# Optimization experiments

Measured on AMD Instinct MI355X. Metric: run time of the kernel, lower is better.

## Reference

```python
import jax, jax.numpy as jnp
import numpy as np

B, T, D = 4, 50, 512
SRC, SENTS, WORDS = 400, 16, 40
NEG = jnp.float32(-1e30)  # stands in for -inf mask fill (numerically identical post-softmax)


def _seq_mask(lengths, max_len):
    # [n, max_len] bool, True where position < length
    return jnp.arange(max_len)[None, :] < lengths[:, None]


def _mlp_score(q, h, Wq, bq, Uc, v):
    # Bahdanau additive score: v^T tanh(W q + U h)
    # q: [b,t,d], h: [b,s,d] -> [b,t,s]
    wq = q @ Wq + bq                       # [b,t,d]
    uh = h @ Uc                            # [b,s,d]
    wquh = jnp.tanh(wq[:, :, None, :] + uh[:, None, :, :])  # [b,t,s,d]
    return jnp.einsum('btsd,d->bts', wquh, v)


def setup_inputs() -> dict:
    key = jax.random.key(0)
    ks = jax.random.split(key, 20)
    s = np.float32(1.0 / np.sqrt(D))
    def p(k, shape):
        return jax.random.normal(k, shape, jnp.float32) * s
    return {
        'source': jax.random.normal(ks[0], (B, T, D), jnp.float32),
        'src_bank': jax.random.normal(ks[1], (SRC, B, D), jnp.float32),
        'src_lengths': jax.random.randint(ks[2], (B,), 1, SRC + 1),
        'qa_sent_bank': jax.random.normal(ks[3], (SENTS, B, D), jnp.float32),
        'qa_sent_lengths': jax.random.randint(ks[4], (B,), 1, SENTS + 1),
        'qa_word_bank': jax.random.normal(ks[5], (WORDS, B, SENTS, D), jnp.float32),
        'qa_word_lengths': jax.random.randint(ks[6], (B, SENTS), 1, WORDS + 1),
        'Wq_word': p(ks[7], (D, D)), 'bq_word': jnp.zeros((D,), jnp.float32),
        'Uc_word': p(ks[8], (D, D)), 'v_word': p(ks[9], (D,)),
        'Wq_sent': p(ks[10], (D, D)), 'bq_sent': jnp.zeros((D,), jnp.float32),
        'Uc_sent': p(ks[11], (D, D)), 'v_sent': p(ks[12], (D,)),
        'Wq_pass': p(ks[13], (D, D)), 'bq_pass': jnp.zeros((D,), jnp.float32),
        'Uc_pass': p(ks[14], (D, D)), 'v_pass': p(ks[15], (D,)),
    }


def _forward(source, src_bank, qa_sent_bank, qa_word_bank,
             Wq_word, bq_word, Uc_word, v_word,
             Wq_sent, bq_sent, Uc_sent, v_sent,
             Wq_pass, bq_pass, Uc_pass, v_pass,
             src_lengths, qa_word_lengths):
    b = source.shape[0]
    # [words,b,sents,d] -> [b,sents,words,d] -> [b, sents*words, d]
    qa_word = jnp.transpose(qa_word_bank, (1, 2, 0, 3)).reshape(b, SENTS * WORDS, D)
    src = jnp.transpose(src_bank, (1, 0, 2))       # [b,src,d]
    sent = jnp.transpose(qa_sent_bank, (1, 0, 2))  # [b,sents,d]

    qa_word_align = _mlp_score(source, qa_word, Wq_word, bq_word, Uc_word, v_word)  # [b,t,sents*words]
    src_align = _mlp_score(source, src, Wq_pass, bq_pass, Uc_pass, v_pass)          # [b,t,src]
    qa_sent_align = _mlp_score(source, sent, Wq_sent, bq_sent, Uc_sent, v_sent)     # [b,t,sents]

    # hierarchical combination: word score scaled by its sentence score
    qa_hier = (qa_word_align.reshape(b, T, SENTS, WORDS)
               * qa_sent_align[..., None]).reshape(b, T, SENTS * WORDS)

    align = jnp.concatenate([src_align, qa_hier], axis=-1)  # [b,t,src+sents*words]

    qa_mask = _seq_mask(qa_word_lengths.reshape(-1), WORDS).reshape(b, SENTS * WORDS)[:, None, :]
    src_mask = _seq_mask(src_lengths, SRC)[:, None, :]
    mask = jnp.concatenate([src_mask, qa_mask], axis=-1)

    align = jnp.where(mask, align, NEG)
    align_vectors = jax.nn.softmax(align, axis=-1)  # joint length-masked softmax

    memory = jnp.concatenate([src, qa_word], axis=1)          # [b, src+sents*words, d]
    c = jnp.einsum('bts,bsd->btd', align_vectors, memory)     # weighted context sum
    return c


def reference(source, src_bank, src_lengths, qa_sent_bank, qa_sent_lengths,
              qa_word_bank, qa_word_lengths,
              Wq_word, bq_word, Uc_word, v_word,
              Wq_sent, bq_sent, Uc_sent, v_sent,
              Wq_pass, bq_pass, Uc_pass, v_pass):
    # qa_sent_lengths is accepted but unused, matching the original forward()
    return _forward(source, src_bank, qa_sent_bank, qa_word_bank,
                    Wq_word, bq_word, Uc_word, v_word,
                    Wq_sent, bq_sent, Uc_sent, v_sent,
                    Wq_pass, bq_pass, Uc_pass, v_pass,
                    src_lengths, qa_word_lengths)
```

## Files before the change

kernel.cpp:

```cpp
#include <hip/hip_runtime.h>
#include <hip/hip_bf16.h>


#define B_    4
#define T_    50
#define D_    512
#define SRC_  400
#define SENTS_ 16
#define WORDS_ 40
#define NW_   640
#define NMEM_ 1040
#define NK_   1056
#define NJOB_ 1056

#define C2L2E 2.8853900817779268f

typedef unsigned short ushort_t;
using s8v = __attribute__((ext_vector_type(8))) short;
using f4v = __attribute__((ext_vector_type(4))) float;

#define OFF_WQ_WORD 0
#define OFF_WQ_SENT 102400
#define OFF_WQ_PASS 204800
#define OFF_UH_SRC  307200
#define OFF_UH_WORD 1126400
#define OFF_UH_SENT 2437120
#define OFF_SC_SRC  2469888
#define OFF_SC_WORD 2549888
#define OFF_SC_SENT 2677888
#define P_BYTE_OFF  10724352ull
#define MT_BYTE_OFF 11265024ull
#define WT_BYTE_OFF 15590400ull

__device__ __forceinline__ ushort_t f2b(float f) {
    __hip_bfloat16 h = __float2bfloat16(f);
    return *(ushort_t*)&h;
}

__global__ __launch_bounds__(256) void k0f_transpose(
    const float* __restrict__ w0, const float* __restrict__ w1,
    const float* __restrict__ w2, const float* __restrict__ w3,
    const float* __restrict__ w4, const float* __restrict__ w5,
    const float* __restrict__ src_bank, const float* __restrict__ qa_word_bank,
    ushort_t* __restrict__ wt, ushort_t* __restrict__ mt)
{
    __shared__ float tile[32][33];
    int bid = blockIdx.x;
    int tx = threadIdx.x & 31, ty = threadIdx.x >> 5;
    if (bid < 1536) {
        int z = bid >> 8, r = bid & 255;
        int n0 = (r & 15) * 32, k0 = (r >> 4) * 32;
        const float* W;
        switch (z) {
            case 0: W = w0; break; case 1: W = w1; break; case 2: W = w2; break;
            case 3: W = w3; break; case 4: W = w4; break; default: W = w5; break;
        }
        ushort_t* Wt = wt + z * (D_ * D_);
#pragma unroll
        for (int a = 0; a < 4; ++a)
            tile[ty + a * 8][tx] = W[(k0 + ty + a * 8) * D_ + n0 + tx];
        __syncthreads();
#pragma unroll
        for (int a = 0; a < 4; ++a)
            Wt[(n0 + ty + a * 8) * D_ + k0 + tx] = f2b(tile[tx][ty + a * 8]);
    } else {
        int tb = bid - 1536;
        int b = tb / 528, r = tb - b * 528;
        int s0 = (r % 33) * 32, d0 = (r / 33) * 32;
#pragma unroll
        for (int a = 0; a < 4; ++a) {
            int s = s0 + ty + a * 8;
            float val = 0.f;
            if (s < SRC_) {
                val = src_bank[(s * B_ + b) * D_ + d0 + tx];
            } else if (s < NMEM_) {
                int j = s - SRC_; int se = j / WORDS_; int wd = j - se * WORDS_;
                val = qa_word_bank[((wd * B_ + b) * SENTS_ + se) * D_ + d0 + tx];
            }
            tile[ty + a * 8][tx] = val;
        }
        __syncthreads();
        ushort_t* base = mt + (size_t)b * D_ * NK_;
#pragma unroll
        for (int a = 0; a < 4; ++a) {
            int d = d0 + ty + a * 8;
            base[(size_t)d * NK_ + s0 + tx] = f2b(tile[tx][ty + a * 8]);
        }
    }
}

__global__ __launch_bounds__(256) void k1_gemm(
    const float* __restrict__ source, const float* __restrict__ src_bank,
    const float* __restrict__ qa_sent_bank, const float* __restrict__ qa_word_bank,
    const ushort_t* __restrict__ wt,
    const float* __restrict__ bq_word, const float* __restrict__ bq_sent,
    const float* __restrict__ bq_pass,
    float* __restrict__ wsf)
{
    __shared__ short At[64 * 32];
    __shared__ short Bt[64 * 32];
    int bid = blockIdx.x;
    int z, rem;
    if (bid < 96)       { z = bid >> 5; rem = bid & 31; }
    else if (bid < 416) { z = 3; rem = bid - 96; }
    else if (bid < 616) { z = 4; rem = bid - 416; }
    else                { z = 5; rem = bid - 616; }
    int by = rem >> 3, bx = rem & 7;
    int M, atype; const float* bias; float* C;
    switch (z) {
        case 0: M = 200;  atype = 0; bias = bq_word; C = wsf + OFF_WQ_WORD; break;
        case 1: M = 200;  atype = 0; bias = bq_sent; C = wsf + OFF_WQ_SENT; break;
        case 2: M = 200;  atype = 0; bias = bq_pass; C = wsf + OFF_WQ_PASS; break;
        case 3: M = 2560; atype = 1; bias = nullptr; C = wsf + OFF_UH_WORD; break;
        case 4: M = 1600; atype = 2; bias = nullptr; C = wsf + OFF_UH_SRC;  break;
        default: M = 64;  atype = 3; bias = nullptr; C = wsf + OFF_UH_SENT; break;
    }
    int m0 = by * 64, n0 = bx * 64;
    const ushort_t* W = wt + z * (D_ * D_);

    int tid = threadIdx.x;
    int lane = tid & 63, wv = tid >> 6;
    int quad = lane >> 4, l16 = lane & 15;
    int sm = tid >> 2, koff = (tid & 3) * 8;

    const float* arow = nullptr;
    {
        int r = m0 + sm;
        if (r < M) {
            if (atype == 0) arow = source + r * D_;
            else if (atype == 1) { int b = r / NW_; int j = r - b * NW_;
                                   int se = j / WORDS_; int wd = j - se * WORDS_;
                                   arow = qa_word_bank + ((wd * B_ + b) * SENTS_ + se) * D_; }
            else if (atype == 2) { int b = r / SRC_; int j = r - b * SRC_;
                                   arow = src_bank + (j * B_ + b) * D_; }
            else                 { int b = r >> 4; int s2 = r & 15;
                                   arow = qa_sent_bank + (s2 * B_ + b) * D_; }
        }
    }
    const ushort_t* wrow = W + (n0 + sm) * D_;

    auto loadA = [&](float* r, int kk) {
        if (arow) {
            float4 f0 = *(const float4*)(arow + kk * 32 + koff);
            float4 f1 = *(const float4*)(arow + kk * 32 + koff + 4);
            r[0]=f0.x; r[1]=f0.y; r[2]=f0.z; r[3]=f0.w;
            r[4]=f1.x; r[5]=f1.y; r[6]=f1.z; r[7]=f1.w;
        } else {
#pragma unroll
            for (int i = 0; i < 8; ++i) r[i] = 0.f;
        }
    };

    f4v acc[4] = { {0.f,0.f,0.f,0.f}, {0.f,0.f,0.f,0.f},
                   {0.f,0.f,0.f,0.f}, {0.f,0.f,0.f,0.f} };

    float a0[8], a1[8];
    int4 w0v, w1v;
    loadA(a0, 0); w0v = *(const int4*)(wrow + 0 * 32 + koff);
    loadA(a1, 1); w1v = *(const int4*)(wrow + 1 * 32 + koff);

    for (int kk = 0; kk < 16; ++kk) {
        union { ushort_t u[8]; int4 v; } pk;
#pragma unroll
        for (int i = 0; i < 8; ++i) pk.u[i] = f2b(a0[i]);
        *(int4*)(At + sm * 32 + koff) = pk.v;
        *(int4*)(Bt + sm * 32 + koff) = w0v;
        __syncthreads();
#pragma unroll
        for (int i = 0; i < 8; ++i) a0[i] = a1[i];
        w0v = w1v;
        if (kk < 14) {
            loadA(a1, kk + 2);
            w1v = *(const int4*)(wrow + (kk + 2) * 32 + koff);
        }
        s8v af = *(const s8v*)(At + (wv * 16 + l16) * 32 + quad * 8);
#pragma unroll
        for (int ng = 0; ng < 4; ++ng) {
            s8v bf = *(const s8v*)(Bt + (ng * 16 + l16) * 32 + quad * 8);
            acc[ng] = __builtin_amdgcn_mfma_f32_16x16x32_bf16(af, bf, acc[ng], 0, 0, 0);
        }
        __syncthreads();
    }
#pragma unroll
    for (int ng = 0; ng < 4; ++ng) {
        int col = n0 + ng * 16 + l16;
        float bb = bias ? bias[col] : 0.f;
#pragma unroll
        for (int rr = 0; rr < 4; ++rr) {
            int row = m0 + wv * 16 + quad * 4 + rr;
            if (row < M) C[row * D_ + col] = (acc[ng][rr] + bb) * C2L2E;
        }
    }
}

__global__ __launch_bounds__(256) void k2_scores(
    const float* __restrict__ v_word, const float* __restrict__ v_sent,
    const float* __restrict__ v_pass,
    const int* __restrict__ src_lengths, const int* __restrict__ qa_word_lengths,
    float* __restrict__ wsf)
{
    int lane = threadIdx.x & 63;
    int job2 = blockIdx.x * 4 + (threadIdx.x >> 6);
    int job = job2 >> 1, th = job2 & 1;
    int b = job / NJOB_, slot = job - b * NJOB_;
    const float* uh; const float* v; const float* wq; float* out; int ostride;
    if (slot < SRC_) {
        if (slot >= src_lengths[b]) return;
        uh = wsf + OFF_UH_SRC + (b * SRC_ + slot) * D_;
        v = v_pass; wq = wsf + OFF_WQ_PASS + b * T_ * D_;
        out = wsf + OFF_SC_SRC + b * T_ * SRC_ + slot; ostride = SRC_;
    } else if (slot < NMEM_) {
        int j = slot - SRC_;
        int se = j / WORDS_; int wd = j - se * WORDS_;
        if (wd >= qa_word_lengths[b * SENTS_ + se]) return;
        uh = wsf + OFF_UH_WORD + (b * NW_ + j) * D_;
        v = v_word; wq = wsf + OFF_WQ_WORD + b * T_ * D_;
        out = wsf + OFF_SC_WORD + b * T_ * NW_ + j; ostride = NW_;
    } else {
        int s2 = slot - NMEM_;
        uh = wsf + OFF_UH_SENT + (b * SENTS_ + s2) * D_;
        v = v_sent; wq = wsf + OFF_WQ_SENT + b * T_ * D_;
        out = wsf + OFF_SC_SENT + b * T_ * SENTS_ + s2; ostride = SENTS_;
    }
    int d0 = lane * 8;
    float4 u0 = *(const float4*)(uh + d0);
    float4 u1 = *(const float4*)(uh + d0 + 4);
    float uhr[8] = {u0.x, u0.y, u0.z, u0.w, u1.x, u1.y, u1.z, u1.w};
    float4 v0 = *(const float4*)(v + d0);
    float4 v1 = *(const float4*)(v + d0 + 4);
    float vr[8] = {v0.x, v0.y, v0.z, v0.w, v1.x, v1.y, v1.z, v1.w};

    float vs = ((vr[0] + vr[1]) + (vr[2] + vr[3])) + ((vr[4] + vr[5]) + (vr[6] + vr[7]));
#pragma unroll
    for (int off = 32; off > 0; off >>= 1) vs += __shfl_xor(vs, off, 64);

    const float* wqh = wq + th * 25 * D_;
#pragma unroll 1
    for (int g = 0; g < 5; ++g) {
        float a5[5];
#pragma unroll
        for (int u5 = 0; u5 < 5; ++u5) {
            const float* wr = wqh + (g * 5 + u5) * D_ + d0;
            float4 w0 = *(const float4*)(wr);
            float4 w1 = *(const float4*)(wr + 4);
            float wrr[8] = {w0.x, w0.y, w0.z, w0.w, w1.x, w1.y, w1.z, w1.w};
            float a = 0.f;
#pragma unroll
            for (int j = 0; j < 8; ++j) {
                float e = __builtin_amdgcn_exp2f(wrr[j] + uhr[j]);
                float r = __builtin_amdgcn_rcpf(e + 1.f);
                a = fmaf(vr[j], r, a);
            }
            a5[u5] = a;
        }
#pragma unroll
        for (int off = 32; off > 0; off >>= 1) {
#pragma unroll
            for (int u5 = 0; u5 < 5; ++u5) a5[u5] += __shfl_xor(a5[u5], off, 64);
        }
        if (lane == 0) {
#pragma unroll
            for (int u5 = 0; u5 < 5; ++u5)
                out[(th * 25 + g * 5 + u5) * ostride] = fmaf(-2.f, a5[u5], vs);
        }
    }
}

__global__ __launch_bounds__(256) void k3a_softmax(
    const int* __restrict__ src_lengths, const int* __restrict__ qa_word_lengths,
    const float* __restrict__ wsf, ushort_t* __restrict__ P)
{
    __shared__ float p[NMEM_];
    __shared__ float red[4];
    int tid = threadIdx.x, lane = tid & 63, wv = tid >> 6;
    int bt = blockIdx.x, b = bt / T_, t = bt - b * T_;
    const float* sc_src  = wsf + OFF_SC_SRC  + bt * SRC_;
    const float* sc_word = wsf + OFF_SC_WORD + bt * NW_;
    const float* sc_sent = wsf + OFF_SC_SENT + bt * SENTS_;
    int slen = src_lengths[b];
    float mx = -3.0e38f;
    for (int j = tid; j < NMEM_; j += 256) {
        float val;
        if (j < SRC_) {
            val = (j < slen) ? sc_src[j] : -1e30f;
        } else {
            int jj = j - SRC_; int se = jj / WORDS_; int wd = jj - se * WORDS_;
            float raw = sc_word[jj] * sc_sent[se];
            val = (wd < qa_word_lengths[b * SENTS_ + se]) ? raw : -1e30f;
        }
        p[j] = val;
        mx = fmaxf(mx, val);
    }
#pragma unroll
    for (int off = 32; off > 0; off >>= 1) mx = fmaxf(mx, __shfl_xor(mx, off, 64));
    if (lane == 0) red[wv] = mx;
    __syncthreads();
    mx = fmaxf(fmaxf(red[0], red[1]), fmaxf(red[2], red[3]));
    __syncthreads();
    float lsum = 0.f;
    for (int j = tid; j < NMEM_; j += 256) {
        float e = __expf(p[j] - mx);
        p[j] = e; lsum += e;
    }
#pragma unroll
    for (int off = 32; off > 0; off >>= 1) lsum += __shfl_xor(lsum, off, 64);
    if (lane == 0) red[wv] = lsum;
    __syncthreads();
    float inv = 1.f / (red[0] + red[1] + red[2] + red[3]);
    ushort_t* prow = P + (size_t)(b * 64 + t) * NK_;
    for (int j = tid; j < NK_; j += 256)
        prow[j] = (j < NMEM_) ? f2b(p[j] * inv) : (ushort_t)0;
}

__global__ __launch_bounds__(256) void k3c_gemm(
    const ushort_t* __restrict__ P, const ushort_t* __restrict__ Mt,
    float* __restrict__ out)
{
    __shared__ short At[64 * 32];
    __shared__ short Bt[32 * 32];
    int b = blockIdx.y;
    int n0 = blockIdx.x * 32;
    int tid = threadIdx.x;
    int lane = tid & 63, wv = tid >> 6;
    int quad = lane >> 4, l16 = lane & 15;
    int smA = tid >> 2, koffA = (tid & 3) * 8;
    int smB = tid >> 3, koffB = (tid & 7) * 4;

    const ushort_t* arow = P + (size_t)(b * 64 + smA) * NK_ + koffA;
    const ushort_t* brow = Mt + ((size_t)(b * D_ + n0 + smB)) * NK_ + koffB;

    f4v acc[2] = { {0.f,0.f,0.f,0.f}, {0.f,0.f,0.f,0.f} };

    int4 a0 = *(const int4*)(arow);
    int2 b0 = *(const int2*)(brow);
    int4 a1 = *(const int4*)(arow + 32);
    int2 b1 = *(const int2*)(brow + 32);
    int4 a2 = *(const int4*)(arow + 64);
    int2 b2 = *(const int2*)(brow + 64);

    for (int kk = 0; kk < 33; ++kk) {
        *(int4*)(At + smA * 32 + koffA) = a0;
        *(int2*)(Bt + smB * 32 + koffB) = b0;
        __syncthreads();
        a0 = a1; a1 = a2; b0 = b1; b1 = b2;
        if (kk < 30) {
            a2 = *(const int4*)(arow + (kk + 3) * 32);
            b2 = *(const int2*)(brow + (kk + 3) * 32);
        }
        s8v af = *(const s8v*)(At + (wv * 16 + l16) * 32 + quad * 8);
#pragma unroll
        for (int ng = 0; ng < 2; ++ng) {
            s8v bf = *(const s8v*)(Bt + (ng * 16 + l16) * 32 + quad * 8);
            acc[ng] = __builtin_amdgcn_mfma_f32_16x16x32_bf16(af, bf, acc[ng], 0, 0, 0);
        }
        __syncthreads();
    }
#pragma unroll
    for (int ng = 0; ng < 2; ++ng) {
        int col = n0 + ng * 16 + l16;
#pragma unroll
        for (int rr = 0; rr < 4; ++rr) {
            int row = wv * 16 + quad * 4 + rr;
            if (row < T_) out[(size_t)(b * T_ + row) * D_ + col] = acc[ng][rr];
        }
    }
}

extern "C" void kernel_launch(void* const* d_in, const int* in_sizes, int n_in,
                              void* d_out, int out_size, void* d_ws, size_t ws_size,
                              hipStream_t stream)
{
    (void)in_sizes; (void)n_in; (void)out_size; (void)ws_size;
    const float* source          = (const float*)d_in[0];
    const float* src_bank        = (const float*)d_in[1];
    const int*   src_lengths     = (const int*)d_in[2];
    const float* qa_sent_bank    = (const float*)d_in[3];
    const float* qa_word_bank    = (const float*)d_in[5];
    const int*   qa_word_lengths = (const int*)d_in[6];
    const float* Wq_word = (const float*)d_in[7];
    const float* bq_word = (const float*)d_in[8];
    const float* Uc_word = (const float*)d_in[9];
    const float* v_word  = (const float*)d_in[10];
    const float* Wq_sent = (const float*)d_in[11];
    const float* bq_sent = (const float*)d_in[12];
    const float* Uc_sent = (const float*)d_in[13];
    const float* v_sent  = (const float*)d_in[14];
    const float* Wq_pass = (const float*)d_in[15];
    const float* bq_pass = (const float*)d_in[16];
    const float* Uc_pass = (const float*)d_in[17];
    const float* v_pass  = (const float*)d_in[18];

    float* wsf = (float*)d_ws;
    ushort_t* Pb  = (ushort_t*)((char*)d_ws + P_BYTE_OFF);
    ushort_t* mt  = (ushort_t*)((char*)d_ws + MT_BYTE_OFF);
    ushort_t* wt  = (ushort_t*)((char*)d_ws + WT_BYTE_OFF);
    float* out = (float*)d_out;

    k0f_transpose<<<dim3(3648), dim3(256), 0, stream>>>(
        Wq_word, Wq_sent, Wq_pass, Uc_word, Uc_pass, Uc_sent,
        src_bank, qa_word_bank, wt, mt);
    k1_gemm<<<dim3(624), dim3(256), 0, stream>>>(
        source, src_bank, qa_sent_bank, qa_word_bank, wt,
        bq_word, bq_sent, bq_pass, wsf);
    k2_scores<<<dim3(NJOB_ * 2), dim3(256), 0, stream>>>(
        v_word, v_sent, v_pass, src_lengths, qa_word_lengths, wsf);
    k3a_softmax<<<dim3(200), dim3(256), 0, stream>>>(src_lengths, qa_word_lengths, wsf, Pb);
    k3c_gemm<<<dim3(16, 4), dim3(256), 0, stream>>>(Pb, mt, out);
}
```

Before: 154.7 us.

## Fuse additive-attention scoring with masked softmax into one per-query kernel

Merges the score kernel and the softmax kernel into one kernel with one 512-thread block per (batch, query) row. The Wq vectors and v are held in registers, and each block computes scores for all memory slots straight into shared memory. This removes the global round trip of the score arrays and one launch. The trade-off is that parallelism changes from 2112 blocks parallel over memory slots to 200 blocks parallel over queries. Each uh row is now re-read by 50 blocks instead of once per half-T, which relies on L2 reuse.

```diff
diff --git a/kernel.cpp b/kernel.cpp
--- a/kernel.cpp
+++ b/kernel.cpp
@@ -11,7 +11,6 @@
 #define NW_   640
 #define NMEM_ 1040
 #define NK_   1056
-#define NJOB_ 1056
 
 #define C2L2E 2.8853900817779268f
 
@@ -25,9 +24,6 @@
 #define OFF_UH_SRC  307200
 #define OFF_UH_WORD 1126400
 #define OFF_UH_SENT 2437120
-#define OFF_SC_SRC  2469888
-#define OFF_SC_WORD 2549888
-#define OFF_SC_SENT 2677888
 #define P_BYTE_OFF  10724352ull
 #define MT_BYTE_OFF 11265024ull
 #define WT_BYTE_OFF 15590400ull
@@ -193,112 +189,138 @@
     }
 }
 
-__global__ __launch_bounds__(256) void k2_scores(
+__global__ __launch_bounds__(512) void k2s_scores_softmax(
     const float* __restrict__ v_word, const float* __restrict__ v_sent,
     const float* __restrict__ v_pass,
-    const int* __restrict__ src_lengths, const int* __restrict__ qa_word_lengths,
-    float* __restrict__ wsf)
-{
-    int lane = threadIdx.x & 63;
-    int job2 = blockIdx.x * 4 + (threadIdx.x >> 6);
-    int job = job2 >> 1, th = job2 & 1;
-    int b = job / NJOB_, slot = job - b * NJOB_;
-    const float* uh; const float* v; const float* wq; float* out; int ostride;
-    if (slot < SRC_) {
-        if (slot >= src_lengths[b]) return;
-        uh = wsf + OFF_UH_SRC + (b * SRC_ + slot) * D_;
-        v = v_pass; wq = wsf + OFF_WQ_PASS + b * T_ * D_;
-        out = wsf + OFF_SC_SRC + b * T_ * SRC_ + slot; ostride = SRC_;
-    } else if (slot < NMEM_) {
-        int j = slot - SRC_;
-        int se = j / WORDS_; int wd = j - se * WORDS_;
-        if (wd >= qa_word_lengths[b * SENTS_ + se]) return;
-        uh = wsf + OFF_UH_WORD + (b * NW_ + j) * D_;
-        v = v_word; wq = wsf + OFF_WQ_WORD + b * T_ * D_;
-        out = wsf + OFF_SC_WORD + b * T_ * NW_ + j; ostride = NW_;
-    } else {
-        int s2 = slot - NMEM_;
-        uh = wsf + OFF_UH_SENT + (b * SENTS_ + s2) * D_;
-        v = v_sent; wq = wsf + OFF_WQ_SENT + b * T_ * D_;
-        out = wsf + OFF_SC_SENT + b * T_ * SENTS_ + s2; ostride = SENTS_;
-    }
-    int d0 = lane * 8;
-    float4 u0 = *(const float4*)(uh + d0);
-    float4 u1 = *(const float4*)(uh + d0 + 4);
-    float uhr[8] = {u0.x, u0.y, u0.z, u0.w, u1.x, u1.y, u1.z, u1.w};
-    float4 v0 = *(const float4*)(v + d0);
-    float4 v1 = *(const float4*)(v + d0 + 4);
-    float vr[8] = {v0.x, v0.y, v0.z, v0.w, v1.x, v1.y, v1.z, v1.w};
-
-    float vs = ((vr[0] + vr[1]) + (vr[2] + vr[3])) + ((vr[4] + vr[5]) + (vr[6] + vr[7]));
-#pragma unroll
-    for (int off = 32; off > 0; off >>= 1) vs += __shfl_xor(vs, off, 64);
-
-    const float* wqh = wq + th * 25 * D_;
-#pragma unroll 1
-    for (int g = 0; g < 5; ++g) {
-        float a5[5];
-#pragma unroll
-        for (int u5 = 0; u5 < 5; ++u5) {
-            const float* wr = wqh + (g * 5 + u5) * D_ + d0;
-            float4 w0 = *(const float4*)(wr);
-            float4 w1 = *(const float4*)(wr + 4);
-            float wrr[8] = {w0.x, w0.y, w0.z, w0.w, w1.x, w1.y, w1.z, w1.w};
-            float a = 0.f;
-#pragma unroll
-            for (int j = 0; j < 8; ++j) {
-                float e = __builtin_amdgcn_exp2f(wrr[j] + uhr[j]);
-                float r = __builtin_amdgcn_rcpf(e + 1.f);
-                a = fmaf(vr[j], r, a);
-            }
-            a5[u5] = a;
-        }
-#pragma unroll
-        for (int off = 32; off > 0; off >>= 1) {
-#pragma unroll
-            for (int u5 = 0; u5 < 5; ++u5) a5[u5] += __shfl_xor(a5[u5], off, 64);
-        }
-        if (lane == 0) {
-#pragma unroll
-            for (int u5 = 0; u5 < 5; ++u5)
-                out[(th * 25 + g * 5 + u5) * ostride] = fmaf(-2.f, a5[u5], vs);
-        }
-    }
-}
-
-__global__ __launch_bounds__(256) void k3a_softmax(
     const int* __restrict__ src_lengths, const int* __restrict__ qa_word_lengths,
     const float* __restrict__ wsf, ushort_t* __restrict__ P)
 {
     __shared__ float p[NMEM_];
-    __shared__ float red[4];
+    __shared__ float sentL[SENTS_];
+    __shared__ float red[8];
+    __shared__ int lensL[SENTS_];
     int tid = threadIdx.x, lane = tid & 63, wv = tid >> 6;
     int bt = blockIdx.x, b = bt / T_, t = bt - b * T_;
-    const float* sc_src  = wsf + OFF_SC_SRC  + bt * SRC_;
-    const float* sc_word = wsf + OFF_SC_WORD + bt * NW_;
-    const float* sc_sent = wsf + OFF_SC_SENT + bt * SENTS_;
     int slen = src_lengths[b];
+    int d0 = lane * 8;
+
+    for (int j = tid; j < NMEM_; j += 512) p[j] = -1e30f;
+    if (tid < SENTS_) lensL[tid] = qa_word_lengths[b * SENTS_ + tid];
+
+    float wqp[8], wqw[8], wqs[8], vp[8], vw[8], vs8[8];
+    {
+        const float* qp = wsf + OFF_WQ_PASS + (size_t)bt * D_ + d0;
+        const float* qw = wsf + OFF_WQ_WORD + (size_t)bt * D_ + d0;
+        const float* qs = wsf + OFF_WQ_SENT + (size_t)bt * D_ + d0;
+        float4 f;
+        f = *(const float4*)(qp);     wqp[0]=f.x; wqp[1]=f.y; wqp[2]=f.z; wqp[3]=f.w;
+        f = *(const float4*)(qp + 4); wqp[4]=f.x; wqp[5]=f.y; wqp[6]=f.z; wqp[7]=f.w;
+        f = *(const float4*)(qw);     wqw[0]=f.x; wqw[1]=f.y; wqw[2]=f.z; wqw[3]=f.w;
+        f = *(const float4*)(qw + 4); wqw[4]=f.x; wqw[5]=f.y; wqw[6]=f.z; wqw[7]=f.w;
+        f = *(const float4*)(qs);     wqs[0]=f.x; wqs[1]=f.y; wqs[2]=f.z; wqs[3]=f.w;
+        f = *(const float4*)(qs + 4); wqs[4]=f.x; wqs[5]=f.y; wqs[6]=f.z; wqs[7]=f.w;
+        f = *(const float4*)(v_pass + d0);     vp[0]=f.x; vp[1]=f.y; vp[2]=f.z; vp[3]=f.w;
+        f = *(const float4*)(v_pass + d0 + 4); vp[4]=f.x; vp[5]=f.y; vp[6]=f.z; vp[7]=f.w;
+        f = *(const float4*)(v_word + d0);     vw[0]=f.x; vw[1]=f.y; vw[2]=f.z; vw[3]=f.w;
+        f = *(const float4*)(v_word + d0 + 4); vw[4]=f.x; vw[5]=f.y; vw[6]=f.z; vw[7]=f.w;
+        f = *(const float4*)(v_sent + d0);     vs8[0]=f.x; vs8[1]=f.y; vs8[2]=f.z; vs8[3]=f.w;
+        f = *(const float4*)(v_sent + d0 + 4); vs8[4]=f.x; vs8[5]=f.y; vs8[6]=f.z; vs8[7]=f.w;
+    }
+    float Vp = ((vp[0]+vp[1])+(vp[2]+vp[3])) + ((vp[4]+vp[5])+(vp[6]+vp[7]));
+    float Vw = ((vw[0]+vw[1])+(vw[2]+vw[3])) + ((vw[4]+vw[5])+(vw[6]+vw[7]));
+    float Vs = ((vs8[0]+vs8[1])+(vs8[2]+vs8[3])) + ((vs8[4]+vs8[5])+(vs8[6]+vs8[7]));
+#pragma unroll
+    for (int off = 32; off > 0; off >>= 1) {
+        Vp += __shfl_xor(Vp, off, 64);
+        Vw += __shfl_xor(Vw, off, 64);
+        Vs += __shfl_xor(Vs, off, 64);
+    }
+
+    auto part8 = [&](const float* uh, const float* wq8, const float* v8) -> float {
+        float4 u0 = *(const float4*)(uh);
+        float4 u1 = *(const float4*)(uh + 4);
+        float ur[8] = {u0.x, u0.y, u0.z, u0.w, u1.x, u1.y, u1.z, u1.w};
+        float a = 0.f;
+#pragma unroll
+        for (int j = 0; j < 8; ++j) {
+            float e = __builtin_amdgcn_exp2f(wq8[j] + ur[j]);
+            float r = __builtin_amdgcn_rcpf(e + 1.f);
+            a = fmaf(v8[j], r, a);
+        }
+        return a;
+    };
+
+    {
+        int s0 = wv * 2;
+        const float* uh = wsf + OFF_UH_SENT + (size_t)(b * SENTS_ + s0) * D_ + d0;
+        float a0 = part8(uh, wqs, vs8);
+        float a1 = part8(uh + D_, wqs, vs8);
+#pragma unroll
+        for (int off = 32; off > 0; off >>= 1) {
+            a0 += __shfl_xor(a0, off, 64);
+            a1 += __shfl_xor(a1, off, 64);
+        }
+        if (lane == 0) {
+            sentL[s0]     = fmaf(-2.f, a0, Vs);
+            sentL[s0 + 1] = fmaf(-2.f, a1, Vs);
+        }
+    }
+    __syncthreads();
+
+    for (int c = wv; c < 208; c += 8) {
+        int j0 = c * 5;
+        float a[5];
+        if (j0 < SRC_) {
+            if (j0 >= slen) continue;
+            const float* uh = wsf + OFF_UH_SRC + (size_t)(b * SRC_ + j0) * D_ + d0;
+#pragma unroll
+            for (int u = 0; u < 5; ++u) a[u] = part8(uh + u * D_, wqp, vp);
+#pragma unroll
+            for (int off = 32; off > 0; off >>= 1) {
+#pragma unroll
+                for (int u = 0; u < 5; ++u) a[u] += __shfl_xor(a[u], off, 64);
+            }
+            if (lane == 0) {
+#pragma unroll
+                for (int u = 0; u < 5; ++u)
+                    if (j0 + u < slen) p[j0 + u] = fmaf(-2.f, a[u], Vp);
+            }
+        } else {
+            int jw = j0 - SRC_;
+            int se = jw / WORDS_;
+            int wd0 = jw - se * WORDS_;
+            int lim = lensL[se];
+            if (wd0 >= lim) continue;
+            const float* uh = wsf + OFF_UH_WORD + (size_t)(b * NW_ + jw) * D_ + d0;
+            float sse = sentL[se];
+#pragma unroll
+            for (int u = 0; u < 5; ++u) a[u] = part8(uh + u * D_, wqw, vw);
+#pragma unroll
+            for (int off = 32; off > 0; off >>= 1) {
+#pragma unroll
+                for (int u = 0; u < 5; ++u) a[u] += __shfl_xor(a[u], off, 64);
+            }
+            if (lane == 0) {
+#pragma unroll
+                for (int u = 0; u < 5; ++u)
+                    if (wd0 + u < lim)
+                        p[SRC_ + jw + u] = fmaf(-2.f, a[u], Vw) * sse;
+            }
+        }
+    }
+    __syncthreads();
+
     float mx = -3.0e38f;
-    for (int j = tid; j < NMEM_; j += 256) {
-        float val;
-        if (j < SRC_) {
-            val = (j < slen) ? sc_src[j] : -1e30f;
-        } else {
-            int jj = j - SRC_; int se = jj / WORDS_; int wd = jj - se * WORDS_;
-            float raw = sc_word[jj] * sc_sent[se];
-            val = (wd < qa_word_lengths[b * SENTS_ + se]) ? raw : -1e30f;
-        }
-        p[j] = val;
-        mx = fmaxf(mx, val);
-    }
+    for (int j = tid; j < NMEM_; j += 512) mx = fmaxf(mx, p[j]);
 #pragma unroll
     for (int off = 32; off > 0; off >>= 1) mx = fmaxf(mx, __shfl_xor(mx, off, 64));
     if (lane == 0) red[wv] = mx;
     __syncthreads();
-    mx = fmaxf(fmaxf(red[0], red[1]), fmaxf(red[2], red[3]));
+    mx = fmaxf(fmaxf(fmaxf(red[0], red[1]), fmaxf(red[2], red[3])),
+               fmaxf(fmaxf(red[4], red[5]), fmaxf(red[6], red[7])));
     __syncthreads();
     float lsum = 0.f;
-    for (int j = tid; j < NMEM_; j += 256) {
+    for (int j = tid; j < NMEM_; j += 512) {
         float e = __expf(p[j] - mx);
         p[j] = e; lsum += e;
     }
@@ -306,9 +328,10 @@
     for (int off = 32; off > 0; off >>= 1) lsum += __shfl_xor(lsum, off, 64);
     if (lane == 0) red[wv] = lsum;
     __syncthreads();
-    float inv = 1.f / (red[0] + red[1] + red[2] + red[3]);
+    float inv = 1.f / (((red[0] + red[1]) + (red[2] + red[3])) +
+                       ((red[4] + red[5]) + (red[6] + red[7])));
     ushort_t* prow = P + (size_t)(b * 64 + t) * NK_;
-    for (int j = tid; j < NK_; j += 256)
+    for (int j = tid; j < NK_; j += 512)
         prow[j] = (j < NMEM_) ? f2b(p[j] * inv) : (ushort_t)0;
 }
 
@@ -402,8 +425,7 @@
     k1_gemm<<<dim3(624), dim3(256), 0, stream>>>(
         source, src_bank, qa_sent_bank, qa_word_bank, wt,
         bq_word, bq_sent, bq_pass, wsf);
-    k2_scores<<<dim3(NJOB_ * 2), dim3(256), 0, stream>>>(
-        v_word, v_sent, v_pass, src_lengths, qa_word_lengths, wsf);
-    k3a_softmax<<<dim3(200), dim3(256), 0, stream>>>(src_lengths, qa_word_lengths, wsf, Pb);
+    k2s_scores_softmax<<<dim3(200), dim3(512), 0, stream>>>(
+        v_word, v_sent, v_pass, src_lengths, qa_word_lengths, wsf, Pb);
     k3c_gemm<<<dim3(16, 4), dim3(256), 0, stream>>>(Pb, mt, out);
 }
```

New measurement: 164.4 us. +6.2%, slower.

## Batch four memory slots per wave in scores; split-K final GEMM across waves

Applied to the files above, without the earlier changes.

The score kernel now has each wave handle four consecutive memory slots, so every Wq row loaded from global memory is reused across four uh vectors. The grid shrinks to a quarter of its former size. The final P·M GEMM splits the K dimension across the four waves. Each wave stages its own tiles without block barriers and computes all 64 rows, then partial results are reduced through shared memory. This adds register pressure and a shared-memory reduction in exchange for fewer loads and syncs.

```diff
diff --git a/kernel.cpp b/kernel.cpp
--- a/kernel.cpp
+++ b/kernel.cpp
@@ -11,7 +11,6 @@
 #define NW_   640
 #define NMEM_ 1040
 #define NK_   1056
-#define NJOB_ 1056
 
 #define C2L2E 2.8853900817779268f
 
@@ -200,32 +199,45 @@
     float* __restrict__ wsf)
 {
     int lane = threadIdx.x & 63;
-    int job2 = blockIdx.x * 4 + (threadIdx.x >> 6);
-    int job = job2 >> 1, th = job2 & 1;
-    int b = job / NJOB_, slot = job - b * NJOB_;
-    const float* uh; const float* v; const float* wq; float* out; int ostride;
-    if (slot < SRC_) {
-        if (slot >= src_lengths[b]) return;
-        uh = wsf + OFF_UH_SRC + (b * SRC_ + slot) * D_;
+    int jid = blockIdx.x * 4 + (threadIdx.x >> 6);
+    int b = jid / 528, r = jid - b * 528;
+    int th = r & 1, grp = r >> 1;
+    const float* uhb; const float* v; const float* wq; float* outb; int ostride;
+    int nact;
+    if (grp < 100) {
+        int slot0 = grp * 4;
+        int slen = src_lengths[b];
+        if (slot0 >= slen) return;
+        nact = min(4, slen - slot0);
+        uhb = wsf + OFF_UH_SRC + (size_t)(b * SRC_ + slot0) * D_;
         v = v_pass; wq = wsf + OFF_WQ_PASS + b * T_ * D_;
-        out = wsf + OFF_SC_SRC + b * T_ * SRC_ + slot; ostride = SRC_;
-    } else if (slot < NMEM_) {
-        int j = slot - SRC_;
-        int se = j / WORDS_; int wd = j - se * WORDS_;
-        if (wd >= qa_word_lengths[b * SENTS_ + se]) return;
-        uh = wsf + OFF_UH_WORD + (b * NW_ + j) * D_;
+        outb = wsf + OFF_SC_SRC + b * T_ * SRC_ + slot0; ostride = SRC_;
+    } else if (grp < 260) {
+        int g = grp - 100; int se = g / 10; int wd0 = (g - se * 10) * 4;
+        int lim = qa_word_lengths[b * SENTS_ + se];
+        if (wd0 >= lim) return;
+        nact = min(4, lim - wd0);
+        int jw = se * WORDS_ + wd0;
+        uhb = wsf + OFF_UH_WORD + (size_t)(b * NW_ + jw) * D_;
         v = v_word; wq = wsf + OFF_WQ_WORD + b * T_ * D_;
-        out = wsf + OFF_SC_WORD + b * T_ * NW_ + j; ostride = NW_;
+        outb = wsf + OFF_SC_WORD + b * T_ * NW_ + jw; ostride = NW_;
     } else {
-        int s2 = slot - NMEM_;
-        uh = wsf + OFF_UH_SENT + (b * SENTS_ + s2) * D_;
+        int s0 = (grp - 260) * 4;
+        nact = 4;
+        uhb = wsf + OFF_UH_SENT + (size_t)(b * SENTS_ + s0) * D_;
         v = v_sent; wq = wsf + OFF_WQ_SENT + b * T_ * D_;
-        out = wsf + OFF_SC_SENT + b * T_ * SENTS_ + s2; ostride = SENTS_;
+        outb = wsf + OFF_SC_SENT + b * T_ * SENTS_ + s0; ostride = SENTS_;
     }
     int d0 = lane * 8;
-    float4 u0 = *(const float4*)(uh + d0);
-    float4 u1 = *(const float4*)(uh + d0 + 4);
-    float uhr[8] = {u0.x, u0.y, u0.z, u0.w, u1.x, u1.y, u1.z, u1.w};
+
+    float uhr[4][8];
+#pragma unroll
+    for (int u = 0; u < 4; ++u) {
+        float4 f0 = *(const float4*)(uhb + u * D_ + d0);
+        float4 f1 = *(const float4*)(uhb + u * D_ + d0 + 4);
+        uhr[u][0]=f0.x; uhr[u][1]=f0.y; uhr[u][2]=f0.z; uhr[u][3]=f0.w;
+        uhr[u][4]=f1.x; uhr[u][5]=f1.y; uhr[u][6]=f1.z; uhr[u][7]=f1.w;
+    }
     float4 v0 = *(const float4*)(v + d0);
     float4 v1 = *(const float4*)(v + d0 + 4);
     float vr[8] = {v0.x, v0.y, v0.z, v0.w, v1.x, v1.y, v1.z, v1.w};
@@ -234,34 +246,44 @@
 #pragma unroll
     for (int off = 32; off > 0; off >>= 1) vs += __shfl_xor(vs, off, 64);
 
-    const float* wqh = wq + th * 25 * D_;
+    const float* wqh = wq + th * 25 * D_ + d0;
 #pragma unroll 1
     for (int g = 0; g < 5; ++g) {
-        float a5[5];
-#pragma unroll
-        for (int u5 = 0; u5 < 5; ++u5) {
-            const float* wr = wqh + (g * 5 + u5) * D_ + d0;
+        float a[4][5];
+#pragma unroll
+        for (int t5 = 0; t5 < 5; ++t5) {
+            const float* wr = wqh + (g * 5 + t5) * D_;
             float4 w0 = *(const float4*)(wr);
             float4 w1 = *(const float4*)(wr + 4);
             float wrr[8] = {w0.x, w0.y, w0.z, w0.w, w1.x, w1.y, w1.z, w1.w};
-            float a = 0.f;
-#pragma unroll
-            for (int j = 0; j < 8; ++j) {
-                float e = __builtin_amdgcn_exp2f(wrr[j] + uhr[j]);
-                float r = __builtin_amdgcn_rcpf(e + 1.f);
-                a = fmaf(vr[j], r, a);
+#pragma unroll
+            for (int u = 0; u < 4; ++u) {
+                float acc = 0.f;
+#pragma unroll
+                for (int j = 0; j < 8; ++j) {
+                    float e = __builtin_amdgcn_exp2f(wrr[j] + uhr[u][j]);
+                    float rc = __builtin_amdgcn_rcpf(e + 1.f);
+                    acc = fmaf(vr[j], rc, acc);
+                }
+                a[u][t5] = acc;
             }
-            a5[u5] = a;
         }
 #pragma unroll
         for (int off = 32; off > 0; off >>= 1) {
 #pragma unroll
-            for (int u5 = 0; u5 < 5; ++u5) a5[u5] += __shfl_xor(a5[u5], off, 64);
+            for (int u = 0; u < 4; ++u)
+#pragma unroll
+                for (int t5 = 0; t5 < 5; ++t5)
+                    a[u][t5] += __shfl_xor(a[u][t5], off, 64);
         }
         if (lane == 0) {
 #pragma unroll
-            for (int u5 = 0; u5 < 5; ++u5)
-                out[(th * 25 + g * 5 + u5) * ostride] = fmaf(-2.f, a5[u5], vs);
+            for (int t5 = 0; t5 < 5; ++t5) {
+                int trow = (th * 25 + g * 5 + t5) * ostride;
+#pragma unroll
+                for (int u = 0; u < 4; ++u)
+                    if (u < nact) outb[trow + u] = fmaf(-2.f, a[u][t5], vs);
+            }
         }
     }
 }
@@ -316,53 +338,80 @@
     const ushort_t* __restrict__ P, const ushort_t* __restrict__ Mt,
     float* __restrict__ out)
 {
-    __shared__ short At[64 * 32];
-    __shared__ short Bt[32 * 32];
+    __shared__ short AtW[4][64 * 32];
+    __shared__ short BtW[4][32 * 32];
+    __shared__ float Cred[4][64 * 32];
     int b = blockIdx.y;
     int n0 = blockIdx.x * 32;
     int tid = threadIdx.x;
-    int lane = tid & 63, wv = tid >> 6;
+    int lane = tid & 63, w = tid >> 6;
     int quad = lane >> 4, l16 = lane & 15;
-    int smA = tid >> 2, koffA = (tid & 3) * 8;
-    int smB = tid >> 3, koffB = (tid & 7) * 4;
-
-    const ushort_t* arow = P + (size_t)(b * 64 + smA) * NK_ + koffA;
-    const ushort_t* brow = Mt + ((size_t)(b * D_ + n0 + smB)) * NK_ + koffB;
-
-    f4v acc[2] = { {0.f,0.f,0.f,0.f}, {0.f,0.f,0.f,0.f} };
-
-    int4 a0 = *(const int4*)(arow);
-    int2 b0 = *(const int2*)(brow);
-    int4 a1 = *(const int4*)(arow + 32);
-    int2 b1 = *(const int2*)(brow + 32);
-    int4 a2 = *(const int4*)(arow + 64);
-    int2 b2 = *(const int2*)(brow + 64);
-
-    for (int kk = 0; kk < 33; ++kk) {
-        *(int4*)(At + smA * 32 + koffA) = a0;
-        *(int2*)(Bt + smB * 32 + koffB) = b0;
-        __syncthreads();
-        a0 = a1; a1 = a2; b0 = b1; b1 = b2;
-        if (kk < 30) {
-            a2 = *(const int4*)(arow + (kk + 3) * 32);
-            b2 = *(const int2*)(brow + (kk + 3) * 32);
-        }
-        s8v af = *(const s8v*)(At + (wv * 16 + l16) * 32 + quad * 8);
-#pragma unroll
-        for (int ng = 0; ng < 2; ++ng) {
-            s8v bf = *(const s8v*)(Bt + (ng * 16 + l16) * 32 + quad * 8);
-            acc[ng] = __builtin_amdgcn_mfma_f32_16x16x32_bf16(af, bf, acc[ng], 0, 0, 0);
-        }
-        __syncthreads();
-    }
-#pragma unroll
-    for (int ng = 0; ng < 2; ++ng) {
-        int col = n0 + ng * 16 + l16;
-#pragma unroll
-        for (int rr = 0; rr < 4; ++rr) {
-            int row = wv * 16 + quad * 4 + rr;
-            if (row < T_) out[(size_t)(b * T_ + row) * D_ + col] = acc[ng][rr];
-        }
+
+    int ks = (w == 0) ? 0 : 9 + (w - 1) * 8;
+    int ke = ks + ((w == 0) ? 9 : 8);
+
+    const ushort_t* arow = P + (size_t)(b * 64 + lane) * NK_;
+    const ushort_t* brow = Mt + (size_t)(b * D_ + n0 + (lane >> 1)) * NK_ + (lane & 1) * 16;
+    short* At = AtW[w];
+    short* Bt = BtW[w];
+    short* atd = At + lane * 32;
+    short* btd = Bt + (lane >> 1) * 32 + (lane & 1) * 16;
+
+    f4v acc[4][2];
+#pragma unroll
+    for (int mi = 0; mi < 4; ++mi)
+#pragma unroll
+        for (int ng = 0; ng < 2; ++ng) acc[mi][ng] = f4v{0.f, 0.f, 0.f, 0.f};
+
+    int4 pa0 = *(const int4*)(arow + ks * 32);
+    int4 pa1 = *(const int4*)(arow + ks * 32 + 8);
+    int4 pa2 = *(const int4*)(arow + ks * 32 + 16);
+    int4 pa3 = *(const int4*)(arow + ks * 32 + 24);
+    int4 pb0 = *(const int4*)(brow + ks * 32);
+    int4 pb1 = *(const int4*)(brow + ks * 32 + 8);
+
+    for (int kk = ks; kk < ke; ++kk) {
+        *(int4*)(atd)      = pa0;
+        *(int4*)(atd + 8)  = pa1;
+        *(int4*)(atd + 16) = pa2;
+        *(int4*)(atd + 24) = pa3;
+        *(int4*)(btd)      = pb0;
+        *(int4*)(btd + 8)  = pb1;
+        if (kk + 1 < ke) {
+            pa0 = *(const int4*)(arow + (kk + 1) * 32);
+            pa1 = *(const int4*)(arow + (kk + 1) * 32 + 8);
+            pa2 = *(const int4*)(arow + (kk + 1) * 32 + 16);
+            pa3 = *(const int4*)(arow + (kk + 1) * 32 + 24);
+            pb0 = *(const int4*)(brow + (kk + 1) * 32);
+            pb1 = *(const int4*)(brow + (kk + 1) * 32 + 8);
+        }
+#pragma unroll
+        for (int mi = 0; mi < 4; ++mi) {
+            s8v af = *(const s8v*)(At + (mi * 16 + l16) * 32 + quad * 8);
+#pragma unroll
+            for (int ng = 0; ng < 2; ++ng) {
+                s8v bf = *(const s8v*)(Bt + (ng * 16 + l16) * 32 + quad * 8);
+                acc[mi][ng] = __builtin_amdgcn_mfma_f32_16x16x32_bf16(af, bf, acc[mi][ng], 0, 0, 0);
+            }
+        }
+    }
+
+#pragma unroll
+    for (int mi = 0; mi < 4; ++mi)
+#pragma unroll
+        for (int ng = 0; ng < 2; ++ng)
+#pragma unroll
+            for (int rr = 0; rr < 4; ++rr)
+                Cred[w][(mi * 16 + quad * 4 + rr) * 32 + ng * 16 + l16] = acc[mi][ng][rr];
+    __syncthreads();
+
+    int i0 = tid * 8;
+#pragma unroll
+    for (int e = 0; e < 8; ++e) {
+        int idx = i0 + e;
+        int row = idx >> 5, col = idx & 31;
+        float s = ((Cred[0][idx] + Cred[1][idx]) + (Cred[2][idx] + Cred[3][idx]));
+        if (row < T_) out[(size_t)(b * T_ + row) * D_ + n0 + col] = s;
     }
 }
 
@@ -402,7 +451,7 @@
     k1_gemm<<<dim3(624), dim3(256), 0, stream>>>(
         source, src_bank, qa_sent_bank, qa_word_bank, wt,
         bq_word, bq_sent, bq_pass, wsf);
-    k2_scores<<<dim3(NJOB_ * 2), dim3(256), 0, stream>>>(
+    k2_scores<<<dim3(528), dim3(256), 0, stream>>>(
         v_word, v_sent, v_pass, src_lengths, qa_word_lengths, wsf);
     k3a_softmax<<<dim3(200), dim3(256), 0, stream>>>(src_lengths, qa_word_lengths, wsf, Pb);
     k3c_gemm<<<dim3(16, 4), dim3(256), 0, stream>>>(Pb, mt, out);
```

Measured after the change: 167.7 us. 1.08x slower.

## Stage shared query rows in LDS and process four memory slots per block

Applied to the files above, without the earlier changes.

Regroups the additive-score kernel so each block handles four consecutive memory slots for the same batch and query half. The 25 query rows are copied once into shared memory and reused by the four waves, instead of each wave streaming them from global memory. This cuts redundant L2/global traffic on the wq rows. In exchange, each block uses about 50KB of LDS, which reduces occupancy, and adds a block barrier.

```diff
diff --git a/kernel.cpp b/kernel.cpp
--- a/kernel.cpp
+++ b/kernel.cpp
@@ -11,7 +11,6 @@
 #define NW_   640
 #define NMEM_ 1040
 #define NK_   1056
-#define NJOB_ 1056
 
 #define C2L2E 2.8853900817779268f
 
@@ -199,30 +198,52 @@
     const int* __restrict__ src_lengths, const int* __restrict__ qa_word_lengths,
     float* __restrict__ wsf)
 {
-    int lane = threadIdx.x & 63;
-    int job2 = blockIdx.x * 4 + (threadIdx.x >> 6);
-    int job = job2 >> 1, th = job2 & 1;
-    int b = job / NJOB_, slot = job - b * NJOB_;
-    const float* uh; const float* v; const float* wq; float* out; int ostride;
-    if (slot < SRC_) {
-        if (slot >= src_lengths[b]) return;
-        uh = wsf + OFF_UH_SRC + (b * SRC_ + slot) * D_;
-        v = v_pass; wq = wsf + OFF_WQ_PASS + b * T_ * D_;
-        out = wsf + OFF_SC_SRC + b * T_ * SRC_ + slot; ostride = SRC_;
-    } else if (slot < NMEM_) {
-        int j = slot - SRC_;
-        int se = j / WORDS_; int wd = j - se * WORDS_;
-        if (wd >= qa_word_lengths[b * SENTS_ + se]) return;
-        uh = wsf + OFF_UH_WORD + (b * NW_ + j) * D_;
-        v = v_word; wq = wsf + OFF_WQ_WORD + b * T_ * D_;
-        out = wsf + OFF_SC_WORD + b * T_ * NW_ + j; ostride = NW_;
+    __shared__ float wqL[25 * D_];
+    int tid = threadIdx.x, lane = tid & 63, wv = tid >> 6;
+    int bid = blockIdx.x;
+    int b = bid / 528, r = bid - b * 528;
+    int th = r & 1, grp = r >> 1;
+
+    const float* uhb; const float* v; const float* wqb; float* outb; int ostride;
+    int nact;
+    if (grp < 100) {
+        int slot0 = grp * 4;
+        int slen = src_lengths[b];
+        if (slot0 >= slen) return;
+        nact = min(4, slen - slot0);
+        uhb = wsf + OFF_UH_SRC + (size_t)(b * SRC_ + slot0) * D_;
+        v = v_pass; wqb = wsf + OFF_WQ_PASS + b * T_ * D_;
+        outb = wsf + OFF_SC_SRC + b * T_ * SRC_ + slot0; ostride = SRC_;
+    } else if (grp < 260) {
+        int g = grp - 100; int se = g / 10; int wd0 = (g - se * 10) * 4;
+        int lim = qa_word_lengths[b * SENTS_ + se];
+        if (wd0 >= lim) return;
+        nact = min(4, lim - wd0);
+        int jw = se * WORDS_ + wd0;
+        uhb = wsf + OFF_UH_WORD + (size_t)(b * NW_ + jw) * D_;
+        v = v_word; wqb = wsf + OFF_WQ_WORD + b * T_ * D_;
+        outb = wsf + OFF_SC_WORD + b * T_ * NW_ + jw; ostride = NW_;
     } else {
-        int s2 = slot - NMEM_;
-        uh = wsf + OFF_UH_SENT + (b * SENTS_ + s2) * D_;
-        v = v_sent; wq = wsf + OFF_WQ_SENT + b * T_ * D_;
-        out = wsf + OFF_SC_SENT + b * T_ * SENTS_ + s2; ostride = SENTS_;
-    }
+        int s0 = (grp - 260) * 4;
+        nact = 4;
+        uhb = wsf + OFF_UH_SENT + (size_t)(b * SENTS_ + s0) * D_;
+        v = v_sent; wqb = wsf + OFF_WQ_SENT + b * T_ * D_;
+        outb = wsf + OFF_SC_SENT + b * T_ * SENTS_ + s0; ostride = SENTS_;
+    }
+
+    {
+        const float4* src4 = (const float4*)(wqb + th * 25 * D_);
+        float4* dst4 = (float4*)wqL;
+#pragma unroll
+        for (int i = 0; i < 12; ++i) dst4[tid + i * 256] = src4[tid + i * 256];
+        if (tid < 128) dst4[tid + 3072] = src4[tid + 3072];
+    }
+    __syncthreads();
+
+    int u = wv;
+    if (u >= nact) return;
     int d0 = lane * 8;
+    const float* uh = uhb + u * D_;
     float4 u0 = *(const float4*)(uh + d0);
     float4 u1 = *(const float4*)(uh + d0 + 4);
     float uhr[8] = {u0.x, u0.y, u0.z, u0.w, u1.x, u1.y, u1.z, u1.w};
@@ -234,13 +255,14 @@
 #pragma unroll
     for (int off = 32; off > 0; off >>= 1) vs += __shfl_xor(vs, off, 64);
 
-    const float* wqh = wq + th * 25 * D_;
+    float* outw = outb + u;
+    const float* wl = wqL + d0;
 #pragma unroll 1
     for (int g = 0; g < 5; ++g) {
         float a5[5];
 #pragma unroll
         for (int u5 = 0; u5 < 5; ++u5) {
-            const float* wr = wqh + (g * 5 + u5) * D_ + d0;
+            const float* wr = wl + (g * 5 + u5) * D_;
             float4 w0 = *(const float4*)(wr);
             float4 w1 = *(const float4*)(wr + 4);
             float wrr[8] = {w0.x, w0.y, w0.z, w0.w, w1.x, w1.y, w1.z, w1.w};
@@ -248,8 +270,8 @@
 #pragma unroll
             for (int j = 0; j < 8; ++j) {
                 float e = __builtin_amdgcn_exp2f(wrr[j] + uhr[j]);
-                float r = __builtin_amdgcn_rcpf(e + 1.f);
-                a = fmaf(vr[j], r, a);
+                float rc = __builtin_amdgcn_rcpf(e + 1.f);
+                a = fmaf(vr[j], rc, a);
             }
             a5[u5] = a;
         }
@@ -261,7 +283,7 @@
         if (lane == 0) {
 #pragma unroll
             for (int u5 = 0; u5 < 5; ++u5)
-                out[(th * 25 + g * 5 + u5) * ostride] = fmaf(-2.f, a5[u5], vs);
+                outw[(th * 25 + g * 5 + u5) * ostride] = fmaf(-2.f, a5[u5], vs);
         }
     }
 }
@@ -402,7 +424,7 @@
     k1_gemm<<<dim3(624), dim3(256), 0, stream>>>(
         source, src_bank, qa_sent_bank, qa_word_bank, wt,
         bq_word, bq_sent, bq_pass, wsf);
-    k2_scores<<<dim3(NJOB_ * 2), dim3(256), 0, stream>>>(
+    k2_scores<<<dim3(2112), dim3(256), 0, stream>>>(
         v_word, v_sent, v_pass, src_lengths, qa_word_lengths, wsf);
     k3a_softmax<<<dim3(200), dim3(256), 0, stream>>>(src_lengths, qa_word_lengths, wsf, Pb);
     k3c_gemm<<<dim3(16, 4), dim3(256), 0, stream>>>(Pb, mt, out);
```

Result: no change. 157.4 us (+1.7%).
